# Optimization experiments

Hardware: AMD Instinct MI355X
Metric: run time of the kernel (lower is better)

Reference implementation:

```python
import jax, jax.numpy as jnp
import numpy as np

B, N, H = 16, 4096, 512
TANH_CLIP = 10.0
USE_TANH = True


def setup_inputs() -> dict:
    key = jax.random.key(0)
    k1, k2, k3, k4, k5 = jax.random.split(key, 5)
    stdv = 1.0 / np.sqrt(H)
    features = jax.random.normal(k1, (B, N, 2 * H), dtype=jnp.float32)
    query = jax.random.normal(k2, (B, 1, H), dtype=jnp.float32)
    Wf = jax.random.uniform(k3, (H, 2 * H), dtype=jnp.float32, minval=-stdv, maxval=stdv)
    Wq = jax.random.uniform(k4, (H, H), dtype=jnp.float32, minval=-stdv, maxval=stdv)
    v = jax.random.uniform(k5, (1, 1, H), dtype=jnp.float32, minval=-stdv, maxval=stdv)
    return {"features": features, "query": query, "Wf": Wf, "Wq": Wq, "v": v}


def reference(features, query, Wf, Wq, v):
    # projected_features: [B, N, H] = features [B,N,2H] @ Wf.T [2H,H]
    projected_features = jnp.einsum('bnf,hf->bnh', features, Wf)
    # projected_query: [B, 1, H]
    projected_query = jnp.einsum('bqf,hf->bqh', query, Wq)
    # fused add + tanh + weighted reduction over H with v -> u: [B, 1, N]
    hidden = jnp.tanh(projected_features + projected_query)  # [B, N, H]
    u = jnp.einsum('oih,bnh->bin', v, hidden)  # v [1,1,H] broadcast over batch -> [B,1,N]
    logits = TANH_CLIP * jnp.tanh(u) if USE_TANH else u
    return (projected_features, logits)
```

## Files before the change

### kernel.cpp

```cpp
#include <hip/hip_runtime.h>
#include <hip/hip_bf16.h>
#include <stdint.h>


#define KDIM 1024
#define HDIM 512

typedef short bf16x8 __attribute__((ext_vector_type(8)));
typedef float f32x4  __attribute__((ext_vector_type(4)));

__device__ __forceinline__ float fast_tanh(float x) {
    float ax = fabsf(x);
    float e  = __expf(-2.0f * ax);
    float r  = (1.0f - e) / (1.0f + e);
    return copysignf(r, x);
}

__device__ __forceinline__ short f2bf(float x) {
    __hip_bfloat16 b = __float2bfloat16(x);
    return (short)__builtin_bit_cast(unsigned short, b);
}

__device__ __forceinline__ bf16x8 cvt8(float4 a, float4 b) {
    bf16x8 o;
    o[0] = f2bf(a.x); o[1] = f2bf(a.y); o[2] = f2bf(a.z); o[3] = f2bf(a.w);
    o[4] = f2bf(b.x); o[5] = f2bf(b.y); o[6] = f2bf(b.z); o[7] = f2bf(b.w);
    return o;
}

__global__ void bshuf_kernel(const float* __restrict__ Wf, short* __restrict__ Bsh) {
    const int tid = blockIdx.x * 256 + threadIdx.x;
    const int kt  = tid >> 11;
    const int gg  = (tid >> 6) & 31;
    const int ln  = tid & 63;
    const int fm  = ln & 15, fkg = ln >> 4;
    const int col = gg * 16 + fm;
    const int k0  = kt * 32 + fkg * 8;
    const float* src = Wf + col * KDIM + k0;
    float4 a = *(const float4*)src;
    float4 b = *(const float4*)(src + 4);
    *(bf16x8*)(Bsh + (size_t)tid * 8) = cvt8(a, b);
}

__global__ void pq_kernel(const float* __restrict__ query,
                          const float* __restrict__ Wq,
                          float* __restrict__ pq) {
    const int t = blockIdx.x * blockDim.x + threadIdx.x;
    const int b = t >> 9, h = t & 511;
    const float4* q  = (const float4*)(query + (b << 9));
    const float4* wq = (const float4*)(Wq + ((size_t)h << 9));
    float s = 0.0f;
    #pragma unroll 4
    for (int i = 0; i < 128; ++i) {
        float4 a = q[i], c = wq[i];
        s += a.x * c.x + a.y * c.y + a.z * c.z + a.w * c.w;
    }
    pq[t] = s;
}

__global__ __launch_bounds__(256, 2) void gemm_kernel(
    const float* __restrict__ A, const short* __restrict__ Bsh,
    const float* __restrict__ pq, const float* __restrict__ v,
    float* __restrict__ pf, float* __restrict__ logits)
{
    __shared__ __align__(16) char ldsA[3][8192];
    __shared__ float uls[256];
    const int t    = threadIdx.x;
    const int lane = t & 63;
    const int w    = t >> 6;
    const int fm   = lane & 15;
    const int fkg  = lane >> 4;
    const int Mbase = blockIdx.x * 64;

    int asrc[2], adst[2];
    #pragma unroll
    for (int i = 0; i < 2; ++i) {
        const int idx  = w * 128 + i * 64 + lane;
        const int row  = idx >> 3;
        const int slot = idx & 7;
        asrc[i] = row * 4096 + ((slot ^ (row & 7)) << 4);
        adst[i] = (w * 2 + i) * 1024;
    }
    const char* Ab = (const char*)(A + (size_t)Mbase * KDIM);
    const char* Bb = (const char*)Bsh + ((size_t)(w * 8 * 64) + lane) * 16;

    int ard[4][2];
    #pragma unroll
    for (int f = 0; f < 4; ++f) {
        const int r = f * 16 + fm, c0 = fkg * 2;
        ard[f][0] = r * 128 + (((c0    ) ^ (r & 7)) << 4);
        ard[f][1] = r * 128 + (((c0 + 1) ^ (r & 7)) << 4);
    }

    f32x4 acc[4][8];
    const f32x4 zf = {0.0f, 0.0f, 0.0f, 0.0f};
    #pragma unroll
    for (int f = 0; f < 4; ++f)
        #pragma unroll
        for (int g = 0; g < 8; ++g) acc[f][g] = zf;

    #define STAGE(BUF, KT) do {                                              \
        _Pragma("unroll")                                                    \
        for (int i = 0; i < 2; ++i)                                          \
            __builtin_amdgcn_global_load_lds(                                \
                (const __attribute__((address_space(1))) void*)              \
                    (Ab + asrc[i] + (((KT) & 31) * 128)),                    \
                (__attribute__((address_space(3))) void*)                    \
                    (&ldsA[BUF][adst[i]]),                                   \
                16, 0, 0);                                                   \
    } while (0)

    STAGE(0, 0);

    bf16x8 bfr[8], abf[4];
    int rb = 0, wb = 1;
    #pragma unroll 1
    for (int kt = 0; kt < 32; ++kt) {
        const char* bk = Bb + kt * 32768;
        #pragma unroll
        for (int g = 0; g < 8; ++g)
            bfr[g] = *(const bf16x8*)(bk + g * 1024);
        STAGE(wb, kt + 1);
        asm volatile("s_waitcnt vmcnt(10)" ::: "memory");
        __builtin_amdgcn_s_barrier();
        asm volatile("" ::: "memory");
        const char* base = ldsA[rb];
        #pragma unroll
        for (int f = 0; f < 4; ++f)
            abf[f] = cvt8(*(const float4*)(base + ard[f][0]),
                          *(const float4*)(base + ard[f][1]));
        #pragma unroll
        for (int f = 0; f < 4; ++f)
            #pragma unroll
            for (int g = 0; g < 8; ++g)
                acc[f][g] = __builtin_amdgcn_mfma_f32_16x16x32_bf16(
                    abf[f], bfr[g], acc[f][g], 0, 0, 0);
        rb = (rb == 2) ? 0 : rb + 1;
        wb = (wb == 2) ? 0 : wb + 1;
    }
    #undef STAGE

    __syncthreads();

    const int bidx = Mbase >> 12;
    const float* pqb = pq + (bidx << 9);
    float vv[8], pv[8];
    #pragma unroll
    for (int g = 0; g < 8; ++g) {
        const int c = w * 128 + g * 16 + fm;
        vv[g] = v[c];
        pv[g] = pqb[c];
    }
    #pragma unroll
    for (int f = 0; f < 4; ++f) {
        #pragma unroll
        for (int rr = 0; rr < 4; ++rr) {
            const int rloc = f * 16 + fkg * 4 + rr;
            float* prow = pf + (size_t)(Mbase + rloc) * HDIM + w * 128 + fm;
            float s = 0.0f;
            #pragma unroll
            for (int g = 0; g < 8; ++g) {
                const float val = acc[f][g][rr];
                __builtin_nontemporal_store(val, &prow[g * 16]);
                s += vv[g] * fast_tanh(val + pv[g]);
            }
            s += __shfl_xor(s, 1);
            s += __shfl_xor(s, 2);
            s += __shfl_xor(s, 4);
            s += __shfl_xor(s, 8);
            if (fm == 0) uls[rloc * 4 + w] = s;
        }
    }
    __syncthreads();
    if (t < 64) {
        const float4 p4 = *(const float4*)(uls + t * 4);
        const float u = p4.x + p4.y + p4.z + p4.w;
        logits[Mbase + t] = 10.0f * fast_tanh(u);
    }
}

extern "C" void kernel_launch(void* const* d_in, const int* in_sizes, int n_in,
                              void* d_out, int out_size, void* d_ws, size_t ws_size,
                              hipStream_t stream) {
    const float* features = (const float*)d_in[0];
    const float* query    = (const float*)d_in[1];
    const float* Wf       = (const float*)d_in[2];
    const float* Wq       = (const float*)d_in[3];
    const float* v        = (const float*)d_in[4];

    float* pf     = (float*)d_out;
    float* logits = (float*)d_out + 33554432;

    float* ws_pq  = (float*)d_ws;
    short* ws_bsh = (short*)(ws_pq + 8192);

    bshuf_kernel<<<256, 256, 0, stream>>>(Wf, ws_bsh);
    pq_kernel<<<16, 512, 0, stream>>>(query, Wq, ws_pq);
    gemm_kernel<<<1024, 256, 0, stream>>>(features, ws_bsh, ws_pq, v, pf, logits);
}
```

Measured before the change: 173.6 us.

## Drop LDS staging, load A directly to registers with double-buffered prefetch

Removes the LDS triple-buffer and barriers for the features tile. Each wave now loads its A fragments straight from global memory into registers and converts them to bf16, while register double-buffering prefetches the next k-step for both A and B. The M tile is halved to 32 rows per block, the grid is doubled, and launch bounds are raised to 3 blocks per CU. The four waves of a block now each read the same A rows instead of sharing them, which adds redundant global/L2 traffic, and B is reloaded twice as often across the grid.

```diff
diff --git a/kernel.cpp b/kernel.cpp
--- a/kernel.cpp
+++ b/kernel.cpp
@@ -58,89 +58,73 @@
     pq[t] = s;
 }
 
-__global__ __launch_bounds__(256, 2) void gemm_kernel(
+__global__ __launch_bounds__(256, 3) void gemm_kernel(
     const float* __restrict__ A, const short* __restrict__ Bsh,
     const float* __restrict__ pq, const float* __restrict__ v,
     float* __restrict__ pf, float* __restrict__ logits)
 {
-    __shared__ __align__(16) char ldsA[3][8192];
-    __shared__ float uls[256];
+    __shared__ float uls[128];
     const int t    = threadIdx.x;
     const int lane = t & 63;
     const int w    = t >> 6;
     const int fm   = lane & 15;
     const int fkg  = lane >> 4;
-    const int Mbase = blockIdx.x * 64;
+    const int Mbase = blockIdx.x * 32;
 
-    int asrc[2], adst[2];
-    #pragma unroll
-    for (int i = 0; i < 2; ++i) {
-        const int idx  = w * 128 + i * 64 + lane;
-        const int row  = idx >> 3;
-        const int slot = idx & 7;
-        asrc[i] = row * 4096 + ((slot ^ (row & 7)) << 4);
-        adst[i] = (w * 2 + i) * 1024;
-    }
-    const char* Ab = (const char*)(A + (size_t)Mbase * KDIM);
+    const float* a0 = A + (size_t)(Mbase + fm) * KDIM + fkg * 8;
+    const float* a1 = a0 + 16 * KDIM;
     const char* Bb = (const char*)Bsh + ((size_t)(w * 8 * 64) + lane) * 16;
 
-    int ard[4][2];
-    #pragma unroll
-    for (int f = 0; f < 4; ++f) {
-        const int r = f * 16 + fm, c0 = fkg * 2;
-        ard[f][0] = r * 128 + (((c0    ) ^ (r & 7)) << 4);
-        ard[f][1] = r * 128 + (((c0 + 1) ^ (r & 7)) << 4);
-    }
-
-    f32x4 acc[4][8];
+    f32x4 acc[2][8];
     const f32x4 zf = {0.0f, 0.0f, 0.0f, 0.0f};
     #pragma unroll
-    for (int f = 0; f < 4; ++f)
+    for (int f = 0; f < 2; ++f)
         #pragma unroll
         for (int g = 0; g < 8; ++g) acc[f][g] = zf;
 
-    #define STAGE(BUF, KT) do {                                              \
-        _Pragma("unroll")                                                    \
-        for (int i = 0; i < 2; ++i)                                          \
-            __builtin_amdgcn_global_load_lds(                                \
-                (const __attribute__((address_space(1))) void*)              \
-                    (Ab + asrc[i] + (((KT) & 31) * 128)),                    \
-                (__attribute__((address_space(3))) void*)                    \
-                    (&ldsA[BUF][adst[i]]),                                   \
-                16, 0, 0);                                                   \
+    float4 aFX[4], aFY[4];
+    bf16x8 bX[8], bY[8];
+    bf16x8 abf[2];
+
+    #define LOAD_A(DST, KT) do {                                             \
+        const int k4 = ((KT) & 31) * 8;      \
+        DST[0] = ((const float4*)a0)[k4];                                    \
+        DST[1] = ((const float4*)a0)[k4 + 1];                                \
+        DST[2] = ((const float4*)a1)[k4];                                    \
+        DST[3] = ((const float4*)a1)[k4 + 1];                                \
     } while (0)
 
-    STAGE(0, 0);
+    #define LOAD_B(DST, KT) do {                                             \
+        const char* bk = Bb + (size_t)(((KT) & 31)) * 32768;                 \
+        _Pragma("unroll")                                                    \
+        for (int g = 0; g < 8; ++g)                                          \
+            DST[g] = *(const bf16x8*)(bk + g * 1024);                        \
+    } while (0)
 
-    bf16x8 bfr[8], abf[4];
-    int rb = 0, wb = 1;
+    #define BODY(KT, AC, BC, AN, BN) do {                                    \
+        LOAD_A(AN, (KT) + 1);                                                \
+        LOAD_B(BN, (KT) + 1);                                                \
+        abf[0] = cvt8(AC[0], AC[1]);                                         \
+        abf[1] = cvt8(AC[2], AC[3]);                                         \
+        _Pragma("unroll")                                                    \
+        for (int f = 0; f < 2; ++f)                                          \
+            _Pragma("unroll")                                                \
+            for (int g = 0; g < 8; ++g)                                      \
+                acc[f][g] = __builtin_amdgcn_mfma_f32_16x16x32_bf16(         \
+                    abf[f], BC[g], acc[f][g], 0, 0, 0);                      \
+    } while (0)
+
+    LOAD_A(aFX, 0);
+    LOAD_B(bX, 0);
+
     #pragma unroll 1
-    for (int kt = 0; kt < 32; ++kt) {
-        const char* bk = Bb + kt * 32768;
-        #pragma unroll
-        for (int g = 0; g < 8; ++g)
-            bfr[g] = *(const bf16x8*)(bk + g * 1024);
-        STAGE(wb, kt + 1);
-        asm volatile("s_waitcnt vmcnt(10)" ::: "memory");
-        __builtin_amdgcn_s_barrier();
-        asm volatile("" ::: "memory");
-        const char* base = ldsA[rb];
-        #pragma unroll
-        for (int f = 0; f < 4; ++f)
-            abf[f] = cvt8(*(const float4*)(base + ard[f][0]),
-                          *(const float4*)(base + ard[f][1]));
-        #pragma unroll
-        for (int f = 0; f < 4; ++f)
-            #pragma unroll
-            for (int g = 0; g < 8; ++g)
-                acc[f][g] = __builtin_amdgcn_mfma_f32_16x16x32_bf16(
-                    abf[f], bfr[g], acc[f][g], 0, 0, 0);
-        rb = (rb == 2) ? 0 : rb + 1;
-        wb = (wb == 2) ? 0 : wb + 1;
+    for (int kt2 = 0; kt2 < 16; ++kt2) {
+        BODY(2 * kt2,     aFX, bX, aFY, bY);
+        BODY(2 * kt2 + 1, aFY, bY, aFX, bX);
     }
-    #undef STAGE
-
-    __syncthreads();
+    #undef LOAD_A
+    #undef LOAD_B
+    #undef BODY
 
     const int bidx = Mbase >> 12;
     const float* pqb = pq + (bidx << 9);
@@ -152,7 +136,7 @@
         pv[g] = pqb[c];
     }
     #pragma unroll
-    for (int f = 0; f < 4; ++f) {
+    for (int f = 0; f < 2; ++f) {
         #pragma unroll
         for (int rr = 0; rr < 4; ++rr) {
             const int rloc = f * 16 + fkg * 4 + rr;
@@ -172,7 +156,7 @@
         }
     }
     __syncthreads();
-    if (t < 64) {
+    if (t < 32) {
         const float4 p4 = *(const float4*)(uls + t * 4);
         const float u = p4.x + p4.y + p4.z + p4.w;
         logits[Mbase + t] = 10.0f * fast_tanh(u);
@@ -196,5 +180,5 @@
 
     bshuf_kernel<<<256, 256, 0, stream>>>(Wf, ws_bsh);
     pq_kernel<<<16, 512, 0, stream>>>(query, Wq, ws_pq);
-    gemm_kernel<<<1024, 256, 0, stream>>>(features, ws_bsh, ws_pq, v, pf, logits);
+    gemm_kernel<<<2048, 256, 0, stream>>>(features, ws_bsh, ws_pq, v, pf, logits);
 }
```

Result: slower. 332.9 us (+91.7%).

## Halve GEMM row tile to 32 and deepen A-staging pipeline to four buffers

Applied to the files above, without the earlier changes.

Shrinks each block's M tile from 64 to 32 rows, doubling the grid to 2048 blocks. Launch bounds rise to 3 blocks per CU to allow more resident waves. The A-tile LDS ring grows from three to four buffers with a prefetch distance of two, and the redundant barrier before the epilogue is removed. The aim is more parallelism and better hiding of global-load latency, at the cost of halving reuse of the B fragments, which doubles L2 traffic for the shuffled weights.

```diff
diff --git a/kernel.cpp b/kernel.cpp
--- a/kernel.cpp
+++ b/kernel.cpp
@@ -58,89 +58,75 @@
     pq[t] = s;
 }
 
-__global__ __launch_bounds__(256, 2) void gemm_kernel(
+__global__ __launch_bounds__(256, 3) void gemm_kernel(
     const float* __restrict__ A, const short* __restrict__ Bsh,
     const float* __restrict__ pq, const float* __restrict__ v,
     float* __restrict__ pf, float* __restrict__ logits)
 {
-    __shared__ __align__(16) char ldsA[3][8192];
-    __shared__ float uls[256];
+    __shared__ __align__(16) char ldsA[4][4096];
+    __shared__ float uls[128];
     const int t    = threadIdx.x;
     const int lane = t & 63;
     const int w    = t >> 6;
     const int fm   = lane & 15;
     const int fkg  = lane >> 4;
-    const int Mbase = blockIdx.x * 64;
+    const int Mbase = blockIdx.x * 32;
 
-    int asrc[2], adst[2];
+    const int srow = t >> 3, sp = t & 7;
+    const int asrc = srow * 4096 + ((sp ^ (srow & 7)) << 4);
+    const int adst = t * 16;
+    const char* Ab = (const char*)(A + (size_t)Mbase * KDIM);
+
+    int ard[2][2];
     #pragma unroll
-    for (int i = 0; i < 2; ++i) {
-        const int idx  = w * 128 + i * 64 + lane;
-        const int row  = idx >> 3;
-        const int slot = idx & 7;
-        asrc[i] = row * 4096 + ((slot ^ (row & 7)) << 4);
-        adst[i] = (w * 2 + i) * 1024;
+    for (int f = 0; f < 2; ++f) {
+        const int r = f * 16 + fm;
+        ard[f][0] = r * 128 + (((fkg * 2    ) ^ (r & 7)) << 4);
+        ard[f][1] = r * 128 + (((fkg * 2 + 1) ^ (r & 7)) << 4);
     }
-    const char* Ab = (const char*)(A + (size_t)Mbase * KDIM);
+
     const char* Bb = (const char*)Bsh + ((size_t)(w * 8 * 64) + lane) * 16;
 
-    int ard[4][2];
-    #pragma unroll
-    for (int f = 0; f < 4; ++f) {
-        const int r = f * 16 + fm, c0 = fkg * 2;
-        ard[f][0] = r * 128 + (((c0    ) ^ (r & 7)) << 4);
-        ard[f][1] = r * 128 + (((c0 + 1) ^ (r & 7)) << 4);
-    }
-
-    f32x4 acc[4][8];
+    f32x4 acc[2][8];
     const f32x4 zf = {0.0f, 0.0f, 0.0f, 0.0f};
     #pragma unroll
-    for (int f = 0; f < 4; ++f)
+    for (int f = 0; f < 2; ++f)
         #pragma unroll
         for (int g = 0; g < 8; ++g) acc[f][g] = zf;
 
-    #define STAGE(BUF, KT) do {                                              \
-        _Pragma("unroll")                                                    \
-        for (int i = 0; i < 2; ++i)                                          \
-            __builtin_amdgcn_global_load_lds(                                \
-                (const __attribute__((address_space(1))) void*)              \
-                    (Ab + asrc[i] + (((KT) & 31) * 128)),                    \
-                (__attribute__((address_space(3))) void*)                    \
-                    (&ldsA[BUF][adst[i]]),                                   \
-                16, 0, 0);                                                   \
-    } while (0)
+    #define STAGE(BUF, KT) \
+        __builtin_amdgcn_global_load_lds( \
+            (const __attribute__((address_space(1))) void*)(Ab + asrc + ((KT) & 31) * 128), \
+            (__attribute__((address_space(3))) void*)(&ldsA[BUF][adst]), 16, 0, 0)
 
     STAGE(0, 0);
+    STAGE(1, 1);
 
-    bf16x8 bfr[8], abf[4];
-    int rb = 0, wb = 1;
-    #pragma unroll 1
+    bf16x8 bfr[8], abf[2];
+
+    #pragma unroll 2
     for (int kt = 0; kt < 32; ++kt) {
-        const char* bk = Bb + kt * 32768;
+        const char* bk = Bb + (size_t)kt * 32768;
         #pragma unroll
         for (int g = 0; g < 8; ++g)
             bfr[g] = *(const bf16x8*)(bk + g * 1024);
-        STAGE(wb, kt + 1);
+        STAGE((kt + 2) & 3, kt + 2);
         asm volatile("s_waitcnt vmcnt(10)" ::: "memory");
         __builtin_amdgcn_s_barrier();
         asm volatile("" ::: "memory");
-        const char* base = ldsA[rb];
+        const char* base = ldsA[kt & 3];
         #pragma unroll
-        for (int f = 0; f < 4; ++f)
+        for (int f = 0; f < 2; ++f)
             abf[f] = cvt8(*(const float4*)(base + ard[f][0]),
                           *(const float4*)(base + ard[f][1]));
         #pragma unroll
-        for (int f = 0; f < 4; ++f)
+        for (int f = 0; f < 2; ++f)
             #pragma unroll
             for (int g = 0; g < 8; ++g)
                 acc[f][g] = __builtin_amdgcn_mfma_f32_16x16x32_bf16(
                     abf[f], bfr[g], acc[f][g], 0, 0, 0);
-        rb = (rb == 2) ? 0 : rb + 1;
-        wb = (wb == 2) ? 0 : wb + 1;
     }
     #undef STAGE
-
-    __syncthreads();
 
     const int bidx = Mbase >> 12;
     const float* pqb = pq + (bidx << 9);
@@ -152,7 +138,7 @@
         pv[g] = pqb[c];
     }
     #pragma unroll
-    for (int f = 0; f < 4; ++f) {
+    for (int f = 0; f < 2; ++f) {
         #pragma unroll
         for (int rr = 0; rr < 4; ++rr) {
             const int rloc = f * 16 + fkg * 4 + rr;
@@ -172,7 +158,7 @@
         }
     }
     __syncthreads();
-    if (t < 64) {
+    if (t < 32) {
         const float4 p4 = *(const float4*)(uls + t * 4);
         const float u = p4.x + p4.y + p4.z + p4.w;
         logits[Mbase + t] = 10.0f * fast_tanh(u);
@@ -196,5 +182,5 @@
 
     bshuf_kernel<<<256, 256, 0, stream>>>(Wf, ws_bsh);
     pq_kernel<<<16, 512, 0, stream>>>(query, Wq, ws_pq);
-    gemm_kernel<<<1024, 256, 0, stream>>>(features, ws_bsh, ws_pq, v, pf, logits);
+    gemm_kernel<<<2048, 256, 0, stream>>>(features, ws_bsh, ws_pq, v, pf, logits);
 }
```

Result: slower. 191.8 us (+10.5%).

## Use 128-row blocks of 8 waves with 4-stage A pipeline and register prefetch

Applied to the files above, without the earlier changes.

The GEMM block grows from 64 to 128 rows and from 4 to 8 waves arranged as 2x4, so each B fragment loaded from global memory serves twice as many rows. The A staging ring goes from 3 to 4 LDS buffers of 16KB with a prefetch distance of two tiles. The LDS-to-register load and bf16 conversion of the next A tile are now interleaved with the current tile's MFMAs through ping-pong register sets. The cost is higher LDS use (64KB per block), more register pressure, and half as many blocks, which may hurt occupancy and load balance.

```diff
diff --git a/kernel.cpp b/kernel.cpp
--- a/kernel.cpp
+++ b/kernel.cpp
@@ -58,39 +58,41 @@
     pq[t] = s;
 }
 
-__global__ __launch_bounds__(256, 2) void gemm_kernel(
+__global__ __launch_bounds__(512, 2) void gemm_kernel(
     const float* __restrict__ A, const short* __restrict__ Bsh,
     const float* __restrict__ pq, const float* __restrict__ v,
     float* __restrict__ pf, float* __restrict__ logits)
 {
-    __shared__ __align__(16) char ldsA[3][8192];
-    __shared__ float uls[256];
+    __shared__ __align__(16) char ldsA[4][16384];
+    __shared__ float uls[512];
     const int t    = threadIdx.x;
     const int lane = t & 63;
     const int w    = t >> 6;
+    const int wm   = w >> 2;
+    const int wn   = w & 3;
     const int fm   = lane & 15;
     const int fkg  = lane >> 4;
-    const int Mbase = blockIdx.x * 64;
+    const int Mbase = blockIdx.x * 128;
 
     int asrc[2], adst[2];
     #pragma unroll
     for (int i = 0; i < 2; ++i) {
-        const int idx  = w * 128 + i * 64 + lane;
-        const int row  = idx >> 3;
-        const int slot = idx & 7;
+        const int c = i * 512 + t;
+        const int row = c >> 3, slot = c & 7;
         asrc[i] = row * 4096 + ((slot ^ (row & 7)) << 4);
-        adst[i] = (w * 2 + i) * 1024;
+        adst[i] = c * 16;
     }
     const char* Ab = (const char*)(A + (size_t)Mbase * KDIM);
-    const char* Bb = (const char*)Bsh + ((size_t)(w * 8 * 64) + lane) * 16;
 
     int ard[4][2];
     #pragma unroll
     for (int f = 0; f < 4; ++f) {
-        const int r = f * 16 + fm, c0 = fkg * 2;
-        ard[f][0] = r * 128 + (((c0    ) ^ (r & 7)) << 4);
-        ard[f][1] = r * 128 + (((c0 + 1) ^ (r & 7)) << 4);
-    }
+        const int r = wm * 64 + f * 16 + fm;
+        ard[f][0] = r * 128 + (((fkg * 2    ) ^ (r & 7)) << 4);
+        ard[f][1] = r * 128 + (((fkg * 2 + 1) ^ (r & 7)) << 4);
+    }
+
+    const char* Bb = (const char*)Bsh + (size_t)((wn * 8 * 64) + lane) * 16;
 
     f32x4 acc[4][8];
     const f32x4 zf = {0.0f, 0.0f, 0.0f, 0.0f};
@@ -104,50 +106,70 @@
         for (int i = 0; i < 2; ++i)                                          \
             __builtin_amdgcn_global_load_lds(                                \
                 (const __attribute__((address_space(1))) void*)              \
-                    (Ab + asrc[i] + (((KT) & 31) * 128)),                    \
+                    (Ab + asrc[i] + ((KT) & 31) * 128),                      \
                 (__attribute__((address_space(3))) void*)                    \
-                    (&ldsA[BUF][adst[i]]),                                   \
-                16, 0, 0);                                                   \
+                    (&ldsA[BUF][adst[i]]), 16, 0, 0);                        \
     } while (0)
 
+    #define BODY(KT, AC, AN) do {                                            \
+        bf16x8 bfr[8];                                                       \
+        const char* bk = Bb + (size_t)(KT) * 32768;                          \
+        _Pragma("unroll")                                                    \
+        for (int g = 0; g < 8; ++g) bfr[g] = *(const bf16x8*)(bk + g * 1024);\
+        asm volatile("" ::: "memory");       \
+        STAGE(((KT) + 2) & 3, (KT) + 2);                                     \
+        asm volatile("s_waitcnt vmcnt(10)" ::: "memory");                    \
+        __builtin_amdgcn_s_barrier();                                        \
+        asm volatile("" ::: "memory");                                       \
+        const char* base = ldsA[((KT) + 1) & 3];                             \
+        float4 ra[8];                                                        \
+        _Pragma("unroll")                                                    \
+        for (int f = 0; f < 4; ++f) {                                        \
+            ra[2 * f]     = *(const float4*)(base + ard[f][0]);              \
+            ra[2 * f + 1] = *(const float4*)(base + ard[f][1]);              \
+        }                                                                    \
+        _Pragma("unroll")                                                    \
+        for (int f = 0; f < 4; ++f)                                          \
+            _Pragma("unroll")                                                \
+            for (int g = 0; g < 8; ++g)                                      \
+                acc[f][g] = __builtin_amdgcn_mfma_f32_16x16x32_bf16(         \
+                    AC[f], bfr[g], acc[f][g], 0, 0, 0);                      \
+        _Pragma("unroll")                                                    \
+        for (int f = 0; f < 4; ++f) AN[f] = cvt8(ra[2 * f], ra[2 * f + 1]);  \
+    } while (0)
+
     STAGE(0, 0);
-
-    bf16x8 bfr[8], abf[4];
-    int rb = 0, wb = 1;
+    STAGE(1, 1);
+    asm volatile("s_waitcnt vmcnt(2)" ::: "memory");
+    __builtin_amdgcn_s_barrier();
+    asm volatile("" ::: "memory");
+    bf16x8 aX[4], aY[4];
+    {
+        const char* base = ldsA[0];
+        float4 ra[8];
+        #pragma unroll
+        for (int f = 0; f < 4; ++f) {
+            ra[2 * f]     = *(const float4*)(base + ard[f][0]);
+            ra[2 * f + 1] = *(const float4*)(base + ard[f][1]);
+        }
+        #pragma unroll
+        for (int f = 0; f < 4; ++f) aX[f] = cvt8(ra[2 * f], ra[2 * f + 1]);
+    }
+
     #pragma unroll 1
-    for (int kt = 0; kt < 32; ++kt) {
-        const char* bk = Bb + kt * 32768;
-        #pragma unroll
-        for (int g = 0; g < 8; ++g)
-            bfr[g] = *(const bf16x8*)(bk + g * 1024);
-        STAGE(wb, kt + 1);
-        asm volatile("s_waitcnt vmcnt(10)" ::: "memory");
-        __builtin_amdgcn_s_barrier();
-        asm volatile("" ::: "memory");
-        const char* base = ldsA[rb];
-        #pragma unroll
-        for (int f = 0; f < 4; ++f)
-            abf[f] = cvt8(*(const float4*)(base + ard[f][0]),
-                          *(const float4*)(base + ard[f][1]));
-        #pragma unroll
-        for (int f = 0; f < 4; ++f)
-            #pragma unroll
-            for (int g = 0; g < 8; ++g)
-                acc[f][g] = __builtin_amdgcn_mfma_f32_16x16x32_bf16(
-                    abf[f], bfr[g], acc[f][g], 0, 0, 0);
-        rb = (rb == 2) ? 0 : rb + 1;
-        wb = (wb == 2) ? 0 : wb + 1;
-    }
+    for (int kt2 = 0; kt2 < 16; ++kt2) {
+        BODY(2 * kt2,     aX, aY);
+        BODY(2 * kt2 + 1, aY, aX);
+    }
+    #undef BODY
     #undef STAGE
-
-    __syncthreads();
 
     const int bidx = Mbase >> 12;
     const float* pqb = pq + (bidx << 9);
     float vv[8], pv[8];
     #pragma unroll
     for (int g = 0; g < 8; ++g) {
-        const int c = w * 128 + g * 16 + fm;
+        const int c = wn * 128 + g * 16 + fm;
         vv[g] = v[c];
         pv[g] = pqb[c];
     }
@@ -155,8 +177,8 @@
     for (int f = 0; f < 4; ++f) {
         #pragma unroll
         for (int rr = 0; rr < 4; ++rr) {
-            const int rloc = f * 16 + fkg * 4 + rr;
-            float* prow = pf + (size_t)(Mbase + rloc) * HDIM + w * 128 + fm;
+            const int rloc = wm * 64 + f * 16 + fkg * 4 + rr;
+            float* prow = pf + (size_t)(Mbase + rloc) * HDIM + wn * 128 + fm;
             float s = 0.0f;
             #pragma unroll
             for (int g = 0; g < 8; ++g) {
@@ -168,11 +190,11 @@
             s += __shfl_xor(s, 2);
             s += __shfl_xor(s, 4);
             s += __shfl_xor(s, 8);
-            if (fm == 0) uls[rloc * 4 + w] = s;
+            if (fm == 0) uls[rloc * 4 + wn] = s;
         }
     }
     __syncthreads();
-    if (t < 64) {
+    if (t < 128) {
         const float4 p4 = *(const float4*)(uls + t * 4);
         const float u = p4.x + p4.y + p4.z + p4.w;
         logits[Mbase + t] = 10.0f * fast_tanh(u);
@@ -196,5 +218,5 @@
 
     bshuf_kernel<<<256, 256, 0, stream>>>(Wf, ws_bsh);
     pq_kernel<<<16, 512, 0, stream>>>(query, Wq, ws_pq);
-    gemm_kernel<<<1024, 256, 0, stream>>>(features, ws_bsh, ws_pq, v, pf, logits);
-}
+    gemm_kernel<<<512, 512, 0, stream>>>(features, ws_bsh, ws_pq, v, pf, logits);
+}
```

New measurement: 184.7 us. 6.4% more time.
